# Kernel optimization log

Measured on AMD Instinct MI355X. Metric: run time of the kernel, lower is better.

## Reference

```python
import jax, jax.numpy as jnp
import numpy as np

N = 50000   # nodes
E = 800000  # directed edges
D = 128     # input_channels


def _kaiming(key, shape):
    fan_in = shape[0]
    return jax.random.normal(key, shape, jnp.float32) * np.float32(np.sqrt(2.0 / fan_in))


def setup_inputs():
    key = jax.random.key(0)
    ks = jax.random.split(key, 8)
    x = jax.random.normal(ks[0], (N, D), jnp.float32)
    edge_index = jax.random.randint(ks[1], (2, E), 0, N, dtype=jnp.int32)
    return {
        "x": x,
        "edge_index": edge_index,
        "W_in": _kaiming(ks[2], (D, D)),      "b_in": jnp.zeros((D,), jnp.float32),
        "W1": _kaiming(ks[3], (D, 2 * D)),    "b1": jnp.zeros((2 * D,), jnp.float32),
        "W2": _kaiming(ks[4], (2 * D, D)),    "b2": jnp.zeros((D,), jnp.float32),
        "W3": _kaiming(ks[5], (D, D // 2)),   "b3": jnp.zeros((D // 2,), jnp.float32),
        "W_out": _kaiming(ks[6], (D // 2, 1)), "b_out": jnp.zeros((1,), jnp.float32),
    }


def _gcn_conv(x, src, dst, W, b, n):
    """PyG GCNConv: add self-loops, symmetric D^-1/2 (A+I) D^-1/2 normalization."""
    h = x @ W  # [n, out]
    loop = jnp.arange(n, dtype=src.dtype)
    s = jnp.concatenate([src, loop])  # message sources (x_j)
    d = jnp.concatenate([dst, loop])  # aggregation targets (x_i)
    deg = jax.ops.segment_sum(jnp.ones_like(d, jnp.float32), d, num_segments=n)
    dis = jnp.where(deg > 0, jax.lax.rsqrt(jnp.maximum(deg, 1.0)), 0.0)
    norm = dis[s] * dis[d]  # [E+n]
    msg = h[s] * norm[:, None]  # gather + scale
    out = jax.ops.segment_sum(msg, d, num_segments=n)  # scatter-add
    return out + b


def reference(x, edge_index, W_in, b_in, W1, b1, W2, b2, W3, b3, W_out, b_out):
    src, dst = edge_index[0], edge_index[1]
    n = x.shape[0]
    lrelu = lambda t: jax.nn.leaky_relu(t, 0.01)
    # dropout in eval mode (identity)
    h = lrelu(x @ W_in + b_in)
    h = lrelu(_gcn_conv(h, src, dst, W1, b1, n))
    h = lrelu(_gcn_conv(h, src, dst, W2, b2, n))
    h = lrelu(_gcn_conv(h, src, dst, W3, b3, n))
    return h @ W_out + b_out  # [n, 1]
```

## Files before the change

### kernel.cpp

```cpp
#include <hip/hip_runtime.h>


#define LRELU(v) ((v) > 0.f ? (v) : 0.01f * (v))

typedef __attribute__((ext_vector_type(8))) _Float16 half8;
typedef __attribute__((ext_vector_type(8))) float float8;
typedef __attribute__((ext_vector_type(4))) float floatx4;

constexpr int CAP = 64;

template <int F>
__device__ __forceinline__ half8 loadB(const float* __restrict__ W, int k0,
                                       int col) {
  half8 h;
#pragma unroll
  for (int j = 0; j < 8; ++j) h[j] = (_Float16)W[(long)(k0 + j) * F + col];
  return h;
}

template <int K, int F, int EPI, typename IT>
__device__ __forceinline__ void gemm_tile(const IT* __restrict__ X,
                                          const float* __restrict__ W,
                                          const float* __restrict__ bias,
                                          const int* __restrict__ cnt,
                                          _Float16* __restrict__ out, int M,
                                          int tile, _Float16* __restrict__ xs) {
  constexpr int TM = 64;
  constexpr int PAD = 8;
  constexpr int LK = K + PAD;
  constexpr int CW = F / 4;
  constexpr int NT = CW / 16;
  constexpr int NK = K / 32;

  const int m0 = tile * TM;
  const int tid = threadIdx.x;
  const int w = tid >> 6;
  const int lane = tid & 63;
  const int m = lane & 15;
  const int q = lane >> 4;

  half8 breg[NT][NK];
#pragma unroll
  for (int t = 0; t < NT; ++t)
#pragma unroll
    for (int kc = 0; kc < NK; ++kc)
      breg[t][kc] = loadB<F>(W, kc * 32 + q * 8, w * CW + t * 16 + m);

  constexpr int CPR = K / 8;
  for (int idx = tid; idx < TM * CPR; idx += 256) {
    const int row = idx / CPR;
    const int kk = idx % CPR;
    const int g = m0 + row;
    half8 h = (half8)(_Float16)0.f;
    if (g < M) {
      if constexpr (sizeof(IT) == 4) {
        const float4* p = (const float4*)&X[(long)g * K + kk * 8];
        float4 a = p[0], cc = p[1];
        h[0] = (_Float16)a.x; h[1] = (_Float16)a.y;
        h[2] = (_Float16)a.z; h[3] = (_Float16)a.w;
        h[4] = (_Float16)cc.x; h[5] = (_Float16)cc.y;
        h[6] = (_Float16)cc.z; h[7] = (_Float16)cc.w;
      } else {
        h = *(const half8*)&X[(long)g * K + kk * 8];
      }
    }
    *(half8*)&xs[row * LK + kk * 8] = h;
  }
  __syncthreads();

  floatx4 acc[4][NT];
#pragma unroll
  for (int rt = 0; rt < 4; ++rt)
#pragma unroll
    for (int t = 0; t < NT; ++t) acc[rt][t] = (floatx4){0.f, 0.f, 0.f, 0.f};

#pragma unroll
  for (int kc = 0; kc < NK; ++kc) {
    half8 af[4];
#pragma unroll
    for (int rt = 0; rt < 4; ++rt)
      af[rt] = *(const half8*)&xs[(rt * 16 + m) * LK + kc * 32 + q * 8];
#pragma unroll
    for (int rt = 0; rt < 4; ++rt)
#pragma unroll
      for (int t = 0; t < NT; ++t)
        acc[rt][t] = __builtin_amdgcn_mfma_f32_16x16x32_f16(af[rt], breg[t][kc],
                                                            acc[rt][t], 0, 0, 0);
  }

#pragma unroll
  for (int rt = 0; rt < 4; ++rt) {
#pragma unroll
    for (int r = 0; r < 4; ++r) {
      const int row = m0 + rt * 16 + q * 4 + r;
      if (row < M) {
        float dv = 1.f;
        if constexpr (EPI == 0 || EPI == 2) dv = rsqrtf((float)cnt[row] + 1.0f);
#pragma unroll
        for (int t = 0; t < NT; ++t) {
          const int col = w * CW + t * 16 + m;
          float v = acc[rt][t][r];
          if constexpr (EPI == 0) { v += bias[col]; v = LRELU(v); v *= dv; }
          if constexpr (EPI == 1) { v += bias[col]; v = LRELU(v); }
          if constexpr (EPI == 2) { v *= dv; }
          out[(long)row * F + col] = (_Float16)v;
        }
      }
    }
  }
}

__global__ __launch_bounds__(256) void k_scat(const int* __restrict__ src,
                                              const int* __restrict__ dst,
                                              int* __restrict__ cnt,
                                              unsigned short* __restrict__ pad,
                                              int E) {
  const int e0 = blockIdx.x * 1024 + (int)threadIdx.x * 4;
  if (e0 + 3 < E) {
    const int4 d4 = *(const int4*)&dst[e0];
    const int4 s4 = *(const int4*)&src[e0];
#pragma unroll
    for (int k = 0; k < 4; ++k) {
      const int d = (&d4.x)[k];
      const int pos = atomicAdd(&cnt[d], 1);
      if (pos < CAP) pad[(long)d * CAP + pos] = (unsigned short)(&s4.x)[k];
    }
  } else {
    for (int e = e0; e < E; ++e) {
      const int d = dst[e];
      const int pos = atomicAdd(&cnt[d], 1);
      if (pos < CAP) pad[(long)d * CAP + pos] = (unsigned short)src[e];
    }
  }
}

__global__ __launch_bounds__(256) void k_gemm1(const float* __restrict__ X,
                                               const float* __restrict__ W,
                                               const float* __restrict__ bias,
                                               const int* __restrict__ cnt,
                                               _Float16* __restrict__ out,
                                               int M) {
  __shared__ _Float16 xs[64 * 136];
  gemm_tile<128, 128, 0, float>(X, W, bias, cnt, out, M, blockIdx.x, xs);
}

__global__ __launch_bounds__(256) void k_gemm3(const _Float16* __restrict__ X,
                                               const float* __restrict__ W3,
                                               const int* __restrict__ cnt,
                                               _Float16* __restrict__ out,
                                               int M) {
  __shared__ _Float16 xs[64 * 136];
  gemm_tile<128, 64, 2, _Float16>(X, W3, nullptr, cnt, out, M, blockIdx.x, xs);
}

__global__ __launch_bounds__(256) void k_g2x(const _Float16* __restrict__ X,
                                             const float* __restrict__ W1,
                                             const float* __restrict__ b1,
                                             const float* __restrict__ W2,
                                             const int* __restrict__ cnt,
                                             _Float16* __restrict__ out, int M) {
  constexpr int LK1 = 128 + 8;
  constexpr int LK2 = 256 + 8;
  __shared__ _Float16 smem[64 * LK2];
  _Float16* xs = smem;
  _Float16* ys = smem;

  const int m0 = blockIdx.x * 64;
  const int tid = threadIdx.x;
  const int w = tid >> 6;
  const int lane = tid & 63;
  const int m = lane & 15;
  const int q = lane >> 4;

  for (int idx = tid; idx < 64 * 16; idx += 256) {
    const int row = idx >> 4;
    const int kk = idx & 15;
    const int g = m0 + row;
    half8 h = (half8)(_Float16)0.f;
    if (g < M) h = *(const half8*)&X[(long)g * 128 + kk * 8];
    *(half8*)&xs[row * LK1 + kk * 8] = h;
  }

  half8 breg1[4][4];
#pragma unroll
  for (int t = 0; t < 4; ++t)
#pragma unroll
    for (int kc = 0; kc < 4; ++kc)
      breg1[t][kc] = loadB<256>(W1, kc * 32 + q * 8, w * 64 + t * 16 + m);

  __syncthreads();

  floatx4 acc1[4][4];
#pragma unroll
  for (int rt = 0; rt < 4; ++rt)
#pragma unroll
    for (int t = 0; t < 4; ++t) acc1[rt][t] = (floatx4){0.f, 0.f, 0.f, 0.f};

#pragma unroll
  for (int kc = 0; kc < 4; ++kc) {
    half8 af[4];
#pragma unroll
    for (int rt = 0; rt < 4; ++rt)
      af[rt] = *(const half8*)&xs[(rt * 16 + m) * LK1 + kc * 32 + q * 8];
#pragma unroll
    for (int rt = 0; rt < 4; ++rt)
#pragma unroll
      for (int t = 0; t < 4; ++t)
        acc1[rt][t] = __builtin_amdgcn_mfma_f32_16x16x32_f16(af[rt], breg1[t][kc],
                                                             acc1[rt][t], 0, 0, 0);
  }

  half8 breg2[2][8];
#pragma unroll
  for (int t = 0; t < 2; ++t)
#pragma unroll
    for (int kc = 0; kc < 8; ++kc)
      breg2[t][kc] = loadB<128>(W2, kc * 32 + q * 8, w * 32 + t * 16 + m);

  __syncthreads();

#pragma unroll
  for (int rt = 0; rt < 4; ++rt) {
#pragma unroll
    for (int r = 0; r < 4; ++r) {
      const int row = rt * 16 + q * 4 + r;
#pragma unroll
      for (int t = 0; t < 4; ++t) {
        const int col = w * 64 + t * 16 + m;
        float v = acc1[rt][t][r] + b1[col];
        ys[row * LK2 + col] = (_Float16)LRELU(v);
      }
    }
  }

  __syncthreads();

  floatx4 acc2[4][2];
#pragma unroll
  for (int rt = 0; rt < 4; ++rt)
#pragma unroll
    for (int t = 0; t < 2; ++t) acc2[rt][t] = (floatx4){0.f, 0.f, 0.f, 0.f};

#pragma unroll
  for (int kc = 0; kc < 8; ++kc) {
    half8 af[4];
#pragma unroll
    for (int rt = 0; rt < 4; ++rt)
      af[rt] = *(const half8*)&ys[(rt * 16 + m) * LK2 + kc * 32 + q * 8];
#pragma unroll
    for (int rt = 0; rt < 4; ++rt)
#pragma unroll
      for (int t = 0; t < 2; ++t)
        acc2[rt][t] = __builtin_amdgcn_mfma_f32_16x16x32_f16(af[rt], breg2[t][kc],
                                                             acc2[rt][t], 0, 0, 0);
  }

#pragma unroll
  for (int rt = 0; rt < 4; ++rt) {
#pragma unroll
    for (int r = 0; r < 4; ++r) {
      const int row = m0 + rt * 16 + q * 4 + r;
      if (row < M) {
        const float dv = rsqrtf((float)cnt[row] + 1.0f);
#pragma unroll
        for (int t = 0; t < 2; ++t) {
          const int col = w * 32 + t * 16 + m;
          out[(long)row * 128 + col] = (_Float16)(acc2[rt][t][r] * dv);
        }
      }
    }
  }
}

__global__ __launch_bounds__(256) void k_agg_pre(const _Float16* __restrict__ G,
                                                 const unsigned short* __restrict__ pad,
                                                 const int* __restrict__ cnt,
                                                 _Float16* __restrict__ out,
                                                 int N, int gHalf) {
  const int b = blockIdx.x;
  const int ph = (b >= gHalf) ? 1 : 0;
  const int blk = b - ph * gHalf;
  const int col0 = ph << 6;

  const int w = threadIdx.x >> 6;
  const int lane = threadIdx.x & 63;
  const int c = lane & 7;
  const int j = lane >> 3;
  const int n = j >> 2;
  const int jj = j & 3;
  int i = blk * 8 + w * 2 + n;
  const bool valid = (i < N);
  if (!valid) i = N - 1;
  const int cni = cnt[i];
  const int cn = min(cni, CAP);
  const float dvi = rsqrtf((float)cni + 1.f);
  const _Float16* gb = G + col0 + c * 8;
  const unsigned short* pl = pad + (long)i * CAP;

  float8 a0 = {0.f, 0.f, 0.f, 0.f, 0.f, 0.f, 0.f, 0.f};
  float8 a1 = a0, a2 = a0, a3 = a0;
  if (jj == 0)
    a0 = __builtin_convertvector(*(const half8*)(gb + (long)i * 128), float8);
  int e = jj;
  for (; e + 12 < cn; e += 16) {
    const int s0 = pl[e], s1 = pl[e + 4], s2 = pl[e + 8], s3 = pl[e + 12];
    a0 += __builtin_convertvector(*(const half8*)(gb + (long)s0 * 128), float8);
    a1 += __builtin_convertvector(*(const half8*)(gb + (long)s1 * 128), float8);
    a2 += __builtin_convertvector(*(const half8*)(gb + (long)s2 * 128), float8);
    a3 += __builtin_convertvector(*(const half8*)(gb + (long)s3 * 128), float8);
  }
  for (; e < cn; e += 4) {
    const int s = pl[e];
    a0 += __builtin_convertvector(*(const half8*)(gb + (long)s * 128), float8);
  }
  a0 += a1 + a2 + a3;
#pragma unroll
  for (int k = 0; k < 8; ++k) {
    a0[k] += __shfl_xor(a0[k], 8);
    a0[k] += __shfl_xor(a0[k], 16);
  }
  if (valid && jj == 0) {
    half8 hv;
#pragma unroll
    for (int k = 0; k < 8; ++k) hv[k] = (_Float16)(a0[k] * dvi);
    *(half8*)&out[(long)i * 128 + col0 + c * 8] = hv;
  }
}

__global__ __launch_bounds__(256) void k_agg_post(const _Float16* __restrict__ G,
                                                  const unsigned short* __restrict__ pad,
                                                  const int* __restrict__ cnt,
                                                  const float* __restrict__ bias,
                                                  _Float16* __restrict__ out,
                                                  int N, int gHalf) {
  const int b = blockIdx.x;
  const int ph = (b >= gHalf) ? 1 : 0;
  const int blk = b - ph * gHalf;
  const int col0 = ph << 6;

  const int w = threadIdx.x >> 6;
  const int lane = threadIdx.x & 63;
  const int c = lane & 7;
  const int j = lane >> 3;
  const int n = j >> 2;
  const int jj = j & 3;
  int i = blk * 8 + w * 2 + n;
  const bool valid = (i < N);
  if (!valid) i = N - 1;
  const int cni = cnt[i];
  const int cn = min(cni, CAP);
  const float dvi = rsqrtf((float)cni + 1.f);
  const _Float16* gb = G + col0 + c * 8;
  const unsigned short* pl = pad + (long)i * CAP;

  float8 a0 = {0.f, 0.f, 0.f, 0.f, 0.f, 0.f, 0.f, 0.f};
  float8 a1 = a0, a2 = a0, a3 = a0;
  if (jj == 0)
    a0 = __builtin_convertvector(*(const half8*)(gb + (long)i * 128), float8);
  int e = jj;
  for (; e + 12 < cn; e += 16) {
    const int s0 = pl[e], s1 = pl[e + 4], s2 = pl[e + 8], s3 = pl[e + 12];
    a0 += __builtin_convertvector(*(const half8*)(gb + (long)s0 * 128), float8);
    a1 += __builtin_convertvector(*(const half8*)(gb + (long)s1 * 128), float8);
    a2 += __builtin_convertvector(*(const half8*)(gb + (long)s2 * 128), float8);
    a3 += __builtin_convertvector(*(const half8*)(gb + (long)s3 * 128), float8);
  }
  for (; e < cn; e += 4) {
    const int s = pl[e];
    a0 += __builtin_convertvector(*(const half8*)(gb + (long)s * 128), float8);
  }
  a0 += a1 + a2 + a3;
#pragma unroll
  for (int k = 0; k < 8; ++k) {
    a0[k] += __shfl_xor(a0[k], 8);
    a0[k] += __shfl_xor(a0[k], 16);
  }
  if (valid && jj == 0) {
    half8 hv;
#pragma unroll
    for (int k = 0; k < 8; ++k) {
      float v = a0[k] * dvi + bias[col0 + c * 8 + k];
      hv[k] = (_Float16)LRELU(v);
    }
    *(half8*)&out[(long)i * 128 + col0 + c * 8] = hv;
  }
}

__global__ __launch_bounds__(256) void k_agg_final(const _Float16* __restrict__ G,
                                                   const unsigned short* __restrict__ pad,
                                                   const int* __restrict__ cnt,
                                                   const float* __restrict__ b3,
                                                   const float* __restrict__ Wout,
                                                   const float* __restrict__ bout,
                                                   float* __restrict__ out, int N) {
  const int w = threadIdx.x >> 6;
  const int lane = threadIdx.x & 63;
  const int c = lane & 7;
  const int j = lane >> 3;
  const int n = j >> 2;
  const int jj = j & 3;
  int i = blockIdx.x * 8 + w * 2 + n;
  const bool valid = (i < N);
  if (!valid) i = N - 1;
  const int cni = cnt[i];
  const int cn = min(cni, CAP);
  const float dvi = rsqrtf((float)cni + 1.f);
  const _Float16* gb = G + c * 8;
  const unsigned short* pl = pad + (long)i * CAP;

  float8 a0 = {0.f, 0.f, 0.f, 0.f, 0.f, 0.f, 0.f, 0.f};
  float8 a1 = a0;
  if (jj == 0)
    a0 = __builtin_convertvector(*(const half8*)(gb + (long)i * 64), float8);
  int e = jj;
  for (; e + 4 < cn; e += 8) {
    const int s0 = pl[e], s1 = pl[e + 4];
    a0 += __builtin_convertvector(*(const half8*)(gb + (long)s0 * 64), float8);
    a1 += __builtin_convertvector(*(const half8*)(gb + (long)s1 * 64), float8);
  }
  if (e < cn)
    a0 += __builtin_convertvector(*(const half8*)(gb + (long)pl[e] * 64), float8);
  a0 += a1;
#pragma unroll
  for (int k = 0; k < 8; ++k) {
    a0[k] += __shfl_xor(a0[k], 8);
    a0[k] += __shfl_xor(a0[k], 16);
  }
  float p = 0.f;
#pragma unroll
  for (int k = 0; k < 8; ++k) {
    const int col = c * 8 + k;
    float v = a0[k] * dvi + b3[col];
    v = LRELU(v);
    p += v * Wout[col];
  }
  p += __shfl_xor(p, 1);
  p += __shfl_xor(p, 2);
  p += __shfl_xor(p, 4);
  if (valid && jj == 0 && c == 0) out[i] = p + bout[0];
}


extern "C" void kernel_launch(void* const* d_in, const int* in_sizes, int n_in,
                              void* d_out, int out_size, void* d_ws, size_t ws_size,
                              hipStream_t stream) {
  const float* x     = (const float*)d_in[0];
  const int* eidx    = (const int*)d_in[1];
  const float* W_in  = (const float*)d_in[2];
  const float* b_in  = (const float*)d_in[3];
  const float* W1    = (const float*)d_in[4];
  const float* b1    = (const float*)d_in[5];
  const float* W2    = (const float*)d_in[6];
  const float* b2    = (const float*)d_in[7];
  const float* W3    = (const float*)d_in[8];
  const float* b3    = (const float*)d_in[9];
  const float* W_out = (const float*)d_in[10];
  const float* b_out = (const float*)d_in[11];
  float* out = (float*)d_out;

  const int N = in_sizes[0] / 128;
  const int E = in_sizes[1] / 2;
  const int* src = eidx;
  const int* dst = eidx + E;

  size_t off = 0;
  char* base = (char*)d_ws;
  auto alloc = [&](size_t bytes) -> void* {
    void* p = base + off;
    off = (off + bytes + 255) & ~(size_t)255;
    return p;
  };
  int* cnt            = (int*)alloc((size_t)N * sizeof(int));
  unsigned short* pad = (unsigned short*)alloc((size_t)N * CAP * 2);
  _Float16* buf1      = (_Float16*)alloc((size_t)N * 128 * 2);
  _Float16* buf2      = (_Float16*)alloc((size_t)N * 128 * 2);
  _Float16* buf3      = (_Float16*)alloc((size_t)N * 64 * 2);

  hipMemsetAsync(cnt, 0, (size_t)N * sizeof(int), stream);

  const int gScat = (E + 1023) / 1024;
  const int gRows = (N + 63) / 64;
  const int gHalf = (N + 7) / 8;
  const int gAggF = (N + 7) / 8;

  k_scat<<<gScat, 256, 0, stream>>>(src, dst, cnt, pad, E);
  k_gemm1<<<gRows, 256, 0, stream>>>(x, W_in, b_in, cnt, buf1, N);
  k_agg_pre<<<2 * gHalf, 256, 0, stream>>>(buf1, pad, cnt, buf2, N, gHalf);
  k_g2x<<<gRows, 256, 0, stream>>>(buf2, W1, b1, W2, cnt, buf1, N);
  k_agg_post<<<2 * gHalf, 256, 0, stream>>>(buf1, pad, cnt, b2, buf2, N, gHalf);
  k_gemm3<<<gRows, 256, 0, stream>>>(buf2, W3, cnt, buf3, N);
  k_agg_final<<<gAggF, 256, 0, stream>>>(buf3, pad, cnt, b3, W_out, b_out,
                                         out, N);
}
```

Before: 294.0 us.

## Partition edge scatter by XCD so each die handles its own destination range

```diff
diff --git a/kernel.cpp b/kernel.cpp
--- a/kernel.cpp
+++ b/kernel.cpp
@@ -6,6 +6,7 @@
 typedef __attribute__((ext_vector_type(8))) _Float16 half8;
 typedef __attribute__((ext_vector_type(8))) float float8;
 typedef __attribute__((ext_vector_type(4))) float floatx4;
+typedef __attribute__((ext_vector_type(4))) int intx4;
 
 constexpr int CAP = 64;
 
@@ -112,24 +113,44 @@
 
 __global__ __launch_bounds__(256) void k_scat(const int* __restrict__ src,
                                               const int* __restrict__ dst,
+                                              int* __restrict__ ctr,
                                               int* __restrict__ cnt,
                                               unsigned short* __restrict__ pad,
-                                              int E) {
-  const int e0 = blockIdx.x * 1024 + (int)threadIdx.x * 4;
-  if (e0 + 3 < E) {
-    const int4 d4 = *(const int4*)&dst[e0];
-    const int4 s4 = *(const int4*)&src[e0];
-#pragma unroll
-    for (int k = 0; k < 4; ++k) {
-      const int d = (&d4.x)[k];
-      const int pos = atomicAdd(&cnt[d], 1);
-      if (pos < CAP) pad[(long)d * CAP + pos] = (unsigned short)(&s4.x)[k];
-    }
-  } else {
-    for (int e = e0; e < E; ++e) {
-      const int d = dst[e];
-      const int pos = atomicAdd(&cnt[d], 1);
-      if (pos < CAP) pad[(long)d * CAP + pos] = (unsigned short)src[e];
+                                              int E, int PR) {
+  int xcd;
+  asm("s_getreg_b32 %0, hwreg(HW_REG_XCC_ID)" : "=s"(xcd));
+  xcd &= 7;
+  const int lo = xcd * PR;
+  const int nCh = (E + 1023) >> 10;
+  const int tid = threadIdx.x;
+  __shared__ int s_ch;
+  for (;;) {
+    if (tid == 0) s_ch = atomicAdd(&ctr[xcd], 1);
+    __syncthreads();
+    const int ch = s_ch;
+    __syncthreads();
+    if (ch >= nCh) break;
+    const int e0 = ch * 1024 + tid * 4;
+    if (e0 + 3 < E) {
+      const intx4 d4 = __builtin_nontemporal_load((const intx4*)&dst[e0]);
+      const intx4 s4 = __builtin_nontemporal_load((const intx4*)&src[e0]);
+#pragma unroll
+      for (int k = 0; k < 4; ++k) {
+        const int d = d4[k];
+        if ((unsigned)(d - lo) < (unsigned)PR) {
+          const int pos = atomicAdd(&cnt[d], 1);
+          if (pos < CAP) pad[(long)d * CAP + pos] = (unsigned short)s4[k];
+        }
+      }
+    } else {
+      const int eEnd = (e0 + 4 < E) ? e0 + 4 : E;
+      for (int e = e0; e < eEnd; ++e) {
+        const int d = dst[e];
+        if ((unsigned)(d - lo) < (unsigned)PR) {
+          const int pos = atomicAdd(&cnt[d], 1);
+          if (pos < CAP) pad[(long)d * CAP + pos] = (unsigned short)src[e];
+        }
+      }
     }
   }
 }
@@ -462,6 +483,7 @@
   const int E = in_sizes[1] / 2;
   const int* src = eidx;
   const int* dst = eidx + E;
+  const int PR = (N + 7) / 8;
 
   size_t off = 0;
   char* base = (char*)d_ws;
@@ -470,20 +492,22 @@
     off = (off + bytes + 255) & ~(size_t)255;
     return p;
   };
+  int* ctr            = (int*)alloc(8 * sizeof(int));
   int* cnt            = (int*)alloc((size_t)N * sizeof(int));
+  const size_t zeroBytes = off;
   unsigned short* pad = (unsigned short*)alloc((size_t)N * CAP * 2);
   _Float16* buf1      = (_Float16*)alloc((size_t)N * 128 * 2);
   _Float16* buf2      = (_Float16*)alloc((size_t)N * 128 * 2);
   _Float16* buf3      = (_Float16*)alloc((size_t)N * 64 * 2);
 
-  hipMemsetAsync(cnt, 0, (size_t)N * sizeof(int), stream);
-
-  const int gScat = (E + 1023) / 1024;
+  hipMemsetAsync(base, 0, zeroBytes, stream);
+
+  const int gScat = 1024;
   const int gRows = (N + 63) / 64;
   const int gHalf = (N + 7) / 8;
   const int gAggF = (N + 7) / 8;
 
-  k_scat<<<gScat, 256, 0, stream>>>(src, dst, cnt, pad, E);
+  k_scat<<<gScat, 256, 0, stream>>>(src, dst, ctr, cnt, pad, E, PR);
   k_gemm1<<<gRows, 256, 0, stream>>>(x, W_in, b_in, cnt, buf1, N);
   k_agg_pre<<<2 * gHalf, 256, 0, stream>>>(buf1, pad, cnt, buf2, N, gHalf);
   k_g2x<<<gRows, 256, 0, stream>>>(buf2, W1, b1, W2, cnt, buf1, N);
```

New measurement: 339.5 us. 15.5% more time.
